# Kernel optimization log

Hardware: AMD Instinct MI355X
Metric: run time of the kernel (lower is better)

## Reference

```python
import jax, jax.numpy as jnp
import numpy as np

B, ND, NK = 4096, 32, 64        # batch, num_drones, num_docks
FD, FK = 16, 16                  # nfeat_drone, nfeat_dock
NHID, H = 128, 4                 # hidden dim, attention heads
ALPHA = 0.2                      # leaky relu slope
NEG = -9e15                      # masking constant from torch code


def setup_inputs() -> dict:
    key = jax.random.key(0)
    ks = jax.random.split(key, 13)
    s = 0.1
    obs = jax.random.normal(ks[0], (B, ND * FD + NK * FK + ND * NK), jnp.float32)
    return {
        "obs": obs,
        # DroneDockGAT params (per-head projections + additive attention vectors)
        "W_drone": jax.random.normal(ks[1], (H, FD, NHID), jnp.float32) * s,
        "W_dock": jax.random.normal(ks[2], (H, FK, NHID), jnp.float32) * s,
        "a_src": jax.random.normal(ks[3], (H, NHID), jnp.float32) * s,
        "a_dst": jax.random.normal(ks[4], (H, NHID), jnp.float32) * s,
        # critic: Linear(nhid*num_drones,64) -> ReLU -> Linear(64,1)
        "Wc1": jax.random.normal(ks[5], (NHID * ND, 64), jnp.float32) * s,
        "bc1": jnp.zeros((64,), jnp.float32),
        "Wc2": jax.random.normal(ks[6], (64, 1), jnp.float32) * s,
        "bc2": jnp.zeros((1,), jnp.float32),
        # actor heads
        "Wad": jax.random.normal(ks[7], (NHID, NHID), jnp.float32) * s,
        "bad": jnp.zeros((NHID,), jnp.float32),
        "Wak": jax.random.normal(ks[8], (NHID, NHID), jnp.float32) * s,
        "bak": jnp.zeros((NHID,), jnp.float32),
    }


def reference(obs, W_drone, W_dock, a_src, a_dst, Wc1, bc1, Wc2, bc2, Wad, bad, Wak, bak):
    sd, sk = ND * FD, NK * FK
    drone = obs[:, :sd].reshape(B, ND, FD)
    dock = obs[:, sd:sd + sk].reshape(B, NK, FK)
    adj = obs[:, sd + sk:].reshape(B, ND, NK)

    # per-head projections: [B, H, ND, NHID] / [B, H, NK, NHID]
    Whd = jnp.einsum('bnf,hfk->bhnk', drone, W_drone)
    Whk = jnp.einsum('bmf,hfk->bhmk', dock, W_dock)

    # additive GAT attention scores e[b,h,n,m]
    e = jax.nn.leaky_relu(
        jnp.einsum('bhnk,hk->bhn', Whd, a_src)[:, :, :, None]
        + jnp.einsum('bhmk,hk->bhm', Whk, a_dst)[:, :, None, :],
        ALPHA,
    )
    e = jnp.where(adj[:, None, :, :] > 0, e, NEG)
    attn = jax.nn.softmax(e, axis=-1)

    # head-averaged outputs with ELU
    h_drone = jax.nn.elu(jnp.einsum('bhnm,bhmk->bnk', attn, Whk) / H)  # [B, ND, NHID]
    h_dock = jax.nn.elu(Whk.mean(axis=1))                               # [B, NK, NHID]

    # critic
    values = jax.nn.relu(h_drone.reshape(B, -1) @ Wc1 + bc1) @ Wc2 + bc2  # [B, 1]

    # actor: masked drone-dock score matrix
    q = h_drone @ Wad + bad
    k = h_dock @ Wak + bak
    scores = jnp.einsum('bnk,bmk->bnm', q, k)
    logits = jnp.where(adj > 0, scores, NEG)  # [B, ND, NK]
    return values, logits
```

## Files before the change

### kernel.cpp

```cpp
#include <hip/hip_runtime.h>
#include <math.h>

#define OBSD 3584
#define NEGC -9e15f

typedef short short8 __attribute__((ext_vector_type(8)));
typedef float float4v __attribute__((ext_vector_type(4)));

#define WS_MT_S   0
#define WS_U_F    8192
#define WS_W_F    8320
#define WS_C0_F   8448
#define WS_AW_F   8452
#define WS_WDMT_S 17160
#define WS_WFT_S  19208

__device__ __forceinline__ float elu_f(float x) {
    return x > 0.f ? x : (__expf(x) - 1.f);
}
__device__ __forceinline__ short f2bf(float f) {
    union { float f; unsigned u; } v; v.f = f;
    unsigned u = v.u;
    unsigned r = (u + 0x7fffu + ((u >> 16) & 1u)) >> 16;
    return (short)r;
}
__device__ __forceinline__ float b2f(short s) {
    union { unsigned u; float f; } v; v.u = ((unsigned)(unsigned short)s) << 16;
    return v.f;
}
__device__ __forceinline__ unsigned pk2(float a, float b) {
    return (unsigned)(unsigned short)f2bf(a) | ((unsigned)(unsigned short)f2bf(b) << 16);
}

__global__ __launch_bounds__(256) void setup_fold(
    const float* __restrict__ W_drone, const float* __restrict__ W_dock,
    const float* __restrict__ a_src, const float* __restrict__ a_dst,
    const float* __restrict__ Wad, const float* __restrict__ Wak,
    const float* __restrict__ bad, const float* __restrict__ bak,
    float* __restrict__ wsf, short* __restrict__ wss)
{
    const int t = threadIdx.x, bi = blockIdx.x;
    if (bi < 16) {
        __shared__ float sa[32 * 132];
        __shared__ float sb[32 * 132];
        const int r0 = (bi >> 2) * 32, i0 = (bi & 3) * 32;
        #pragma unroll
        for (int qq = 0; qq < 4; ++qq) {
            int e = (t + 256 * qq) * 4;
            int r = e >> 7, cc = e & 127;
            *(float4*)&sa[r * 132 + cc] = *(const float4*)&Wad[(r0 + r) * 128 + cc];
            *(float4*)&sb[r * 132 + cc] = *(const float4*)&Wak[(i0 + r) * 128 + cc];
        }
        __syncthreads();
        int rr = (t >> 4) * 2, ii = (t & 15) * 2;
        float a00 = 0.f, a01 = 0.f, a10 = 0.f, a11 = 0.f;
        for (int c = 0; c < 128; ++c) {
            float x0 = sa[rr * 132 + c], x1 = sa[(rr + 1) * 132 + c];
            float y0 = sb[ii * 132 + c], y1 = sb[(ii + 1) * 132 + c];
            a00 += x0 * y0; a01 += x0 * y1; a10 += x1 * y0; a11 += x1 * y1;
        }
        wss[WS_MT_S + (i0 + ii) * 128 + (r0 + rr)]         = f2bf(a00);
        wss[WS_MT_S + (i0 + ii + 1) * 128 + (r0 + rr)]     = f2bf(a01);
        wss[WS_MT_S + (i0 + ii) * 128 + (r0 + rr + 1)]     = f2bf(a10);
        wss[WS_MT_S + (i0 + ii + 1) * 128 + (r0 + rr + 1)] = f2bf(a11);
    } else if (bi == 16) {
        if (t < 128) {
            float acc = 0.f;
            for (int c = 0; c < 128; ++c) acc += Wad[t * 128 + c] * bak[c];
            wsf[WS_U_F + t] = acc;
        } else {
            int j = t - 128;
            float acc = 0.f;
            for (int c = 0; c < 128; ++c) acc += Wak[j * 128 + c] * bad[c];
            wsf[WS_W_F + j] = acc;
        }
        if (t == 0) {
            float acc = 0.f;
            for (int c = 0; c < 128; ++c) acc += bad[c] * bak[c];
            wsf[WS_C0_F] = acc;
        }
    } else {
        if (t < 64) {
            int h = t >> 4, f = t & 15;
            const float* wrow = W_drone + h * 2048 + f * 128;
            const float* arow = a_src + h * 128;
            float acc = 0.f;
            for (int k = 0; k < 128; ++k) acc += wrow[k] * arow[k];
            wsf[WS_AW_F + t] = acc;
        } else if (t < 128) {
            int tt = t - 64;
            int h = tt >> 4, f = tt & 15;
            const float* wrow = W_dock + h * 2048 + f * 128;
            const float* arow = a_dst + h * 128;
            float acc = 0.f;
            for (int k = 0; k < 128; ++k) acc += wrow[k] * arow[k];
            wsf[WS_AW_F + 64 + tt] = acc;
        }
        for (int idx = t; idx < 2048; idx += 256) {
            int k2 = idx >> 4, f = idx & 15;
            float v = 0.25f * (W_dock[f * 128 + k2] + W_dock[2048 + f * 128 + k2]
                             + W_dock[4096 + f * 128 + k2] + W_dock[6144 + f * 128 + k2]);
            wss[WS_WDMT_S + k2 * 16 + f] = f2bf(v);
        }
        for (int idx = t; idx < 8192; idx += 256) {
            int k2 = idx >> 6, f64 = idx & 63;
            float v = W_dock[(f64 >> 4) * 2048 + (f64 & 15) * 128 + k2];
            wss[WS_WFT_S + k2 * 64 + f64] = f2bf(v);
        }
    }
}

__global__ __launch_bounds__(256, 2) void k1_attn_hd(
    const float* __restrict__ obs,
    const float* __restrict__ wsf, const short* __restrict__ wss,
    short* __restrict__ hdg)
{
    __shared__ __align__(16) char sm[57856];
    short* sD   = (short*)(sm + 0);
    short* sK   = (short*)(sm + 1024);
    short* sAdj = (short*)(sm + 3072);
    float* sAw  = (float*)(sm + 7680);
    float* sSrc = (float*)(sm + 8192);
    float* sDst = (float*)(sm + 8704);
    short* sAt  = (short*)(sm + 9728);
    short* sT   = (short*)(sm + 28160);
    short* sHd  = (short*)(sm + 32768);
    short* sWf  = (short*)(sm + 41472);

    const int t = threadIdx.x;
    const int b = blockIdx.x;
    const float* obsrow = obs + (size_t)b * OBSD;
    const int L = t & 63, c = L & 15, q = L >> 4, w = t >> 6;

    #pragma unroll
    for (int i = 0; i < 4; ++i) {
        int q4 = t + 256 * i;
        if (q4 < 896) {
            float4 v = ((const float4*)obsrow)[q4];
            int e0 = q4 * 4;
            if (e0 < 512) {
                int n = e0 >> 4, f0 = e0 & 15;
                sD[(f0 + 0) * 32 + n] = f2bf(v.x);
                sD[(f0 + 1) * 32 + n] = f2bf(v.y);
                sD[(f0 + 2) * 32 + n] = f2bf(v.z);
                sD[(f0 + 3) * 32 + n] = f2bf(v.w);
            } else if (e0 < 1536) {
                int e = e0 - 512;
                int m = e >> 4, f0 = e & 15;
                sK[(f0 + 0) * 64 + m] = f2bf(v.x);
                sK[(f0 + 1) * 64 + m] = f2bf(v.y);
                sK[(f0 + 2) * 64 + m] = f2bf(v.z);
                sK[(f0 + 3) * 64 + m] = f2bf(v.w);
            } else {
                int e = e0 - 1536;
                int n = e >> 6, m0 = e & 63;
                uint2 pkd = { pk2(v.x, v.y), pk2(v.z, v.w) };
                *(uint2*)&sAdj[n * 72 + m0] = pkd;
            }
        }
    }
    #pragma unroll
    for (int i = 0; i < 4; ++i)
        ((uint4*)sWf)[t + 256 * i] = ((const uint4*)(wss + WS_WFT_S))[t + 256 * i];
    if (t < 128) sAw[t] = wsf[WS_AW_F + t];
    __syncthreads();

    if (t < 128) {
        int h = t >> 5, n = t & 31;
        float acc = 0.f;
        #pragma unroll
        for (int f = 0; f < 16; ++f) acc += b2f(sD[f * 32 + n]) * sAw[h * 16 + f];
        sSrc[h * 32 + n] = acc;
    }
    {
        int h = t >> 6, m = t & 63;
        float acc = 0.f;
        #pragma unroll
        for (int f = 0; f < 16; ++f) acc += b2f(sK[f * 64 + m]) * sAw[64 + h * 16 + f];
        sDst[h * 64 + m] = acc;
    }
    __syncthreads();

    {
        int row = t >> 1, j = t & 1;
        int h = row >> 5, n = row & 31, m0 = j * 32;
        float sv = sSrc[h * 32 + n];
        float e32[32];
        float pmax = -INFINITY;
        #pragma unroll
        for (int mm = 0; mm < 32; ++mm) {
            int m = m0 + mm;
            float e = sv + sDst[h * 64 + m];
            e = e > 0.f ? e : 0.2f * e;
            e = (b2f(sAdj[n * 72 + m]) > 0.f) ? e : NEGC;
            e32[mm] = e;
            pmax = fmaxf(pmax, e);
        }
        pmax = fmaxf(pmax, __shfl_xor(pmax, 1, 2));
        float psum = 0.f;
        #pragma unroll
        for (int mm = 0; mm < 32; ++mm) { e32[mm] = __expf(e32[mm] - pmax); psum += e32[mm]; }
        psum += __shfl_xor(psum, 1, 2);
        float rinv = 1.f / psum;
        unsigned* ab = (unsigned*)sAt;
        int ub = (h * 2304 + n * 72 + m0) >> 1;
        #pragma unroll
        for (int mm = 0; mm < 32; mm += 2)
            ab[ub + (mm >> 1)] = pk2(e32[mm] * rinv, e32[mm + 1] * rinv);
    }
    __syncthreads();

    {
        int h = w;
        float4v accT[2] = { {0,0,0,0}, {0,0,0,0} };
        #pragma unroll
        for (int mt = 0; mt < 2; ++mt)
            #pragma unroll
            for (int kq = 0; kq < 2; ++kq) {
                short8 a = *(const short8*)&sAt[h * 2304 + (mt * 16 + c) * 72 + kq * 32 + q * 8];
                short8 bb = *(const short8*)&sK[c * 64 + kq * 32 + q * 8];
                accT[mt] = __builtin_amdgcn_mfma_f32_16x16x32_bf16(a, bb, accT[mt], 0, 0, 0);
            }
        #pragma unroll
        for (int mt = 0; mt < 2; ++mt)
            #pragma unroll
            for (int i = 0; i < 4; ++i)
                sT[(mt * 16 + q * 4 + i) * 72 + h * 16 + c] = f2bf(accT[mt][i]);
    }
    __syncthreads();

    {
        int mt = w & 1, ntb = (w >> 1) * 4;
        float4v acc[4] = { {0,0,0,0}, {0,0,0,0}, {0,0,0,0}, {0,0,0,0} };
        #pragma unroll
        for (int kq = 0; kq < 2; ++kq) {
            short8 a = *(const short8*)&sT[(mt * 16 + c) * 72 + kq * 32 + q * 8];
            #pragma unroll
            for (int p = 0; p < 4; ++p) {
                short8 bb = *(const short8*)&sWf[((ntb + p) * 16 + c) * 64 + kq * 32 + q * 8];
                acc[p] = __builtin_amdgcn_mfma_f32_16x16x32_bf16(a, bb, acc[p], 0, 0, 0);
            }
        }
        #pragma unroll
        for (int p = 0; p < 4; ++p)
            #pragma unroll
            for (int i = 0; i < 4; ++i) {
                float v = elu_f(acc[p][i] * 0.25f);
                sHd[(mt * 16 + q * 4 + i) * 136 + (ntb + p) * 16 + c] = f2bf(v);
            }
    }
    __syncthreads();

    {
        int n = t >> 3, k2 = (t & 7) * 16;
        uint4 x0 = *(const uint4*)&sHd[n * 136 + k2];
        uint4 x1 = *(const uint4*)&sHd[n * 136 + k2 + 8];
        uint4* dst = (uint4*)(hdg + (size_t)b * 4096 + n * 128 + k2);
        dst[0] = x0; dst[1] = x1;
    }
}

__global__ __launch_bounds__(256) void k2_critic(
    const short* __restrict__ hdg,
    const float* __restrict__ Wc1, const float* __restrict__ bc1,
    const float* __restrict__ Wc2, const float* __restrict__ bc2,
    float* __restrict__ out_values)
{
    __shared__ __align__(16) char sm[46592];
    short* As   = (short*)(sm + 0);
    float* Wst  = (float*)(sm + 9216);
    short* Bh   = (short*)(sm + 27648);
    short* Blo  = (short*)(sm + 36864);
    float* bc1L = (float*)(sm + 46080);
    float* wc2L = (float*)(sm + 46336);

    const int t = threadIdx.x;
    const int r0 = blockIdx.x * 64;
    const int L = t & 63, c = L & 15, q = L >> 4, w = t >> 6;

    if (t < 64) { bc1L[t] = bc1[t]; wc2L[t] = Wc2[t]; }

    float4v acc[4] = { {0,0,0,0}, {0,0,0,0}, {0,0,0,0}, {0,0,0,0} };

    for (int kc = 0; kc < 64; ++kc) {
        __syncthreads();
        {
            int r = t >> 2, kk0 = (t & 3) * 16;
            const uint4* src = (const uint4*)(hdg + (size_t)(r0 + r) * 4096 + kc * 64 + kk0);
            *(uint4*)&As[r * 72 + kk0]     = src[0];
            *(uint4*)&As[r * 72 + kk0 + 8] = src[1];
        }
        {
            int el = t >> 2, j0 = (t & 3) * 16;
            const float4* src = (const float4*)&Wc1[(size_t)(kc * 64 + el) * 64 + j0];
            #pragma unroll
            for (int u = 0; u < 4; ++u)
                *(float4*)&Wst[el * 72 + j0 + 4 * u] = src[u];
        }
        __syncthreads();
        {
            int j = t & 63, elb = (t >> 6) * 16;
            #pragma unroll
            for (int e = 0; e < 16; e += 2) {
                float v0 = Wst[(elb + e) * 72 + j];
                float v1 = Wst[(elb + e + 1) * 72 + j];
                short h0 = f2bf(v0), h1 = f2bf(v1);
                float l0 = v0 - b2f(h0), l1 = v1 - b2f(h1);
                *(unsigned*)&Bh[j * 72 + elb + e]  = (unsigned)(unsigned short)h0 | ((unsigned)(unsigned short)h1 << 16);
                *(unsigned*)&Blo[j * 72 + elb + e] = (unsigned)(unsigned short)f2bf(l0) | ((unsigned)(unsigned short)f2bf(l1) << 16);
            }
        }
        __syncthreads();
        #pragma unroll
        for (int kq = 0; kq < 2; ++kq) {
            short8 a = *(const short8*)&As[(w * 16 + c) * 72 + kq * 32 + q * 8];
            #pragma unroll
            for (int ct = 0; ct < 4; ++ct) {
                short8 bh = *(const short8*)&Bh[(ct * 16 + c) * 72 + kq * 32 + q * 8];
                short8 bl = *(const short8*)&Blo[(ct * 16 + c) * 72 + kq * 32 + q * 8];
                acc[ct] = __builtin_amdgcn_mfma_f32_16x16x32_bf16(a, bh, acc[ct], 0, 0, 0);
                acc[ct] = __builtin_amdgcn_mfma_f32_16x16x32_bf16(a, bl, acc[ct], 0, 0, 0);
            }
        }
    }
    float bc2v = bc2[0];
    #pragma unroll
    for (int i = 0; i < 4; ++i) {
        float sv = 0.f;
        #pragma unroll
        for (int ct = 0; ct < 4; ++ct) {
            float pre = acc[ct][i] + bc1L[ct * 16 + c];
            pre = fmaxf(pre, 0.f);
            sv += pre * wc2L[ct * 16 + c];
        }
        sv += __shfl_xor(sv, 1, 16);
        sv += __shfl_xor(sv, 2, 16);
        sv += __shfl_xor(sv, 4, 16);
        sv += __shfl_xor(sv, 8, 16);
        if (c == 0) out_values[r0 + w * 16 + q * 4 + i] = sv + bc2v;
    }
}

__global__ __launch_bounds__(256, 2) void k3_logits(
    const float* __restrict__ obs,
    const float* __restrict__ wsf, const short* __restrict__ wss,
    float* __restrict__ out_logits)
{
    __shared__ __align__(16) char sm[75648];
    short* dockRm = (short*)(sm + 0);
    short* adjBf  = (short*)(sm + 2048);
    short* hdS    = (short*)(sm + 6656);
    short* hkS    = (short*)(sm + 15360);
    short* wdmTS  = (short*)(sm + 32768);
    short* t2S    = (short*)(sm + 32768);
    float* suL    = (float*)(sm + 41472);
    float* swL    = (float*)(sm + 41600);
    float* uL     = (float*)(sm + 41856);
    float* wL     = (float*)(sm + 42368);
    short* MtS    = (short*)(sm + 42880);

    const int t = threadIdx.x;
    const int b = blockIdx.x;
    const float* obsrow = obs + (size_t)b * OBSD;
    short* hdg = (short*)out_logits;
    const int L = t & 63, c = L & 15, q = L >> 4, w = t >> 6;

    {
        int n = t >> 3, k2 = (t & 7) * 16;
        const uint4* src = (const uint4*)(hdg + (size_t)b * 4096 + n * 128 + k2);
        uint4 x0 = src[0], x1 = src[1];
        *(uint4*)&hdS[n * 136 + k2]     = x0;
        *(uint4*)&hdS[n * 136 + k2 + 8] = x1;
    }
    {
        float4 v = ((const float4*)obsrow)[128 + t];
        int m = t >> 2, f0 = (t & 3) * 4;
        uint2 pkd = { pk2(v.x, v.y), pk2(v.z, v.w) };
        *(uint2*)&dockRm[m * 16 + f0] = pkd;
    }
    #pragma unroll
    for (int i = 0; i < 2; ++i) {
        int q4 = 384 + t + 256 * i;
        if (q4 < 896) {
            float4 v = ((const float4*)obsrow)[q4];
            int e = q4 * 4 - 1536;
            int n = e >> 6, m0 = e & 63;
            uint2 pkd = { pk2(v.x, v.y), pk2(v.z, v.w) };
            *(uint2*)&adjBf[n * 72 + m0] = pkd;
        }
    }
    ((uint4*)wdmTS)[t] = ((const uint4*)(wss + WS_WDMT_S))[t];
    #pragma unroll
    for (int i = 0; i < 8; ++i)
        ((uint4*)MtS)[t + 256 * i] = ((const uint4*)(wss + WS_MT_S))[t + 256 * i];
    if (t < 128) uL[t] = wsf[WS_U_F + t];
    else wL[t - 128] = wsf[WS_W_F + (t - 128)];
    __syncthreads();

    {
        int mt = w;
        short8 a;
        if (q < 2) a = *(const short8*)&dockRm[(mt * 16 + c) * 16 + q * 8];
        else a = short8{0, 0, 0, 0, 0, 0, 0, 0};
        float swp[4] = {0.f, 0.f, 0.f, 0.f};
        #pragma unroll
        for (int nt = 0; nt < 8; ++nt) {
            short8 bb;
            if (q < 2) bb = *(const short8*)&wdmTS[(nt * 16 + c) * 16 + q * 8];
            else bb = short8{0, 0, 0, 0, 0, 0, 0, 0};
            float4v acc = {0, 0, 0, 0};
            acc = __builtin_amdgcn_mfma_f32_16x16x32_bf16(a, bb, acc, 0, 0, 0);
            float wv = wL[nt * 16 + c];
            #pragma unroll
            for (int i = 0; i < 4; ++i) {
                float ev = elu_f(acc[i]);
                hkS[(mt * 16 + q * 4 + i) * 136 + nt * 16 + c] = f2bf(ev);
                swp[i] += ev * wv;
            }
        }
        #pragma unroll
        for (int i = 0; i < 4; ++i) {
            float sv = swp[i];
            sv += __shfl_xor(sv, 1, 16);
            sv += __shfl_xor(sv, 2, 16);
            sv += __shfl_xor(sv, 4, 16);
            sv += __shfl_xor(sv, 8, 16);
            if (c == 0) swL[mt * 16 + q * 4 + i] = sv;
        }
    }
    {
        int n = t >> 3, p = t & 7;
        float a = 0.f;
        #pragma unroll
        for (int kk = 0; kk < 16; kk += 2) {
            unsigned uu = *(const unsigned*)&hdS[n * 136 + p * 16 + kk];
            a += b2f((short)(uu & 0xffff)) * uL[p * 16 + kk]
               + b2f((short)(uu >> 16))   * uL[p * 16 + kk + 1];
        }
        a += __shfl_xor(a, 1, 8);
        a += __shfl_xor(a, 2, 8);
        a += __shfl_xor(a, 4, 8);
        if (p == 0) suL[n] = a;
    }
    __syncthreads();

    {
        int mt = w & 1, ntb = (w >> 1) * 4;
        float4v acc[4] = { {0,0,0,0}, {0,0,0,0}, {0,0,0,0}, {0,0,0,0} };
        #pragma unroll
        for (int kq = 0; kq < 4; ++kq) {
            short8 a = *(const short8*)&hdS[(mt * 16 + c) * 136 + kq * 32 + q * 8];
            #pragma unroll
            for (int p = 0; p < 4; ++p) {
                short8 bb = *(const short8*)&MtS[((ntb + p) * 16 + c) * 128 + kq * 32 + q * 8];
                acc[p] = __builtin_amdgcn_mfma_f32_16x16x32_bf16(a, bb, acc[p], 0, 0, 0);
            }
        }
        __syncthreads();
        #pragma unroll
        for (int p = 0; p < 4; ++p)
            #pragma unroll
            for (int i = 0; i < 4; ++i)
                t2S[(mt * 16 + q * 4 + i) * 136 + (ntb + p) * 16 + c] = f2bf(acc[p][i]);
    }
    __syncthreads();

    {
        const float c0v = wsf[WS_C0_F];
        int ntd = w;
        float* lg = out_logits + (size_t)b * 2048;
        #pragma unroll
        for (int mt = 0; mt < 2; ++mt) {
            float4v acc = {0, 0, 0, 0};
            #pragma unroll
            for (int kq = 0; kq < 4; ++kq) {
                short8 a  = *(const short8*)&t2S[(mt * 16 + c) * 136 + kq * 32 + q * 8];
                short8 bb = *(const short8*)&hkS[(ntd * 16 + c) * 136 + kq * 32 + q * 8];
                acc = __builtin_amdgcn_mfma_f32_16x16x32_bf16(a, bb, acc, 0, 0, 0);
            }
            int col = ntd * 16 + c;
            float swv = swL[col];
            #pragma unroll
            for (int i = 0; i < 4; ++i) {
                int row = mt * 16 + q * 4 + i;
                float val = acc[i] + suL[row] + swv + c0v;
                bool keep = b2f(adjBf[row * 72 + col]) > 0.f;
                lg[row * 64 + col] = keep ? val : NEGC;
            }
        }
    }
}

extern "C" void kernel_launch(void* const* d_in, const int* in_sizes, int n_in,
                              void* d_out, int out_size, void* d_ws, size_t ws_size,
                              hipStream_t stream) {
    (void)in_sizes; (void)n_in; (void)out_size; (void)ws_size;
    const float* obs     = (const float*)d_in[0];
    const float* W_drone = (const float*)d_in[1];
    const float* W_dock  = (const float*)d_in[2];
    const float* a_src   = (const float*)d_in[3];
    const float* a_dst   = (const float*)d_in[4];
    const float* Wc1     = (const float*)d_in[5];
    const float* bc1     = (const float*)d_in[6];
    const float* Wc2     = (const float*)d_in[7];
    const float* bc2     = (const float*)d_in[8];
    const float* Wad     = (const float*)d_in[9];
    const float* bad     = (const float*)d_in[10];
    const float* Wak     = (const float*)d_in[11];
    const float* bak     = (const float*)d_in[12];
    float* out = (float*)d_out;
    float* wsf = (float*)d_ws;
    short* wss = (short*)d_ws;
    short* hdg = (short*)(out + 4096);

    setup_fold<<<dim3(18), dim3(256), 0, stream>>>(
        W_drone, W_dock, a_src, a_dst, Wad, Wak, bad, bak, wsf, wss);
    k1_attn_hd<<<dim3(4096), dim3(256), 0, stream>>>(obs, wsf, wss, hdg);
    k2_critic<<<dim3(64), dim3(256), 0, stream>>>(hdg, Wc1, bc1, Wc2, bc2, out);
    k3_logits<<<dim3(4096), dim3(256), 0, stream>>>(obs, wsf, wss, out + 4096);
}
```

Measured before the change: 309.9 us.

## Pre-split Wc1 into bf16 hi/lo and widen critic GEMM grid

Adds a setup kernel that transposes Wc1 and splits it into bf16 high and low parts in workspace. A new critic kernel uses 256 blocks of 16 rows each instead of 64 blocks and runs two MFMAs per step (hi and lo) to keep near-fp32 accuracy. The goal is better GPU occupancy for the critic GEMM and dropping on-the-fly fp32 weight conversion. The new path is taken only when the workspace is large enough, otherwise the old kernel runs.

```diff
diff --git a/kernel.cpp b/kernel.cpp
--- a/kernel.cpp
+++ b/kernel.cpp
@@ -14,6 +14,9 @@
 #define WS_AW_F   8452
 #define WS_WDMT_S 17160
 #define WS_WFT_S  19208
+#define WS_WC1H_S 32768
+#define WS_WC1L_S 294912
+#define WS_NEED_BYTES 1114112ull
 
 __device__ __forceinline__ float elu_f(float x) {
     return x > 0.f ? x : (__expf(x) - 1.f);
@@ -107,6 +110,20 @@
             float v = W_dock[(f64 >> 4) * 2048 + (f64 & 15) * 128 + k2];
             wss[WS_WFT_S + k2 * 64 + f64] = f2bf(v);
         }
+    }
+}
+
+__global__ __launch_bounds__(256) void setup_wc1(
+    const float* __restrict__ Wc1,
+    short* __restrict__ wc1h, short* __restrict__ wc1l)
+{
+    const int col = blockIdx.x;
+    for (int k = threadIdx.x; k < 4096; k += 256) {
+        float v = Wc1[(size_t)k * 64 + col];
+        short hi = f2bf(v);
+        float lo = v - b2f(hi);
+        wc1h[col * 4096 + k] = hi;
+        wc1l[col * 4096 + k] = f2bf(lo);
     }
 }
 
@@ -341,6 +358,74 @@
     }
 }
 
+__global__ __launch_bounds__(256) void k2_critic2(
+    const short* __restrict__ hdg,
+    const short* __restrict__ wc1h, const short* __restrict__ wc1l,
+    const float* __restrict__ bc1,
+    const float* __restrict__ Wc2, const float* __restrict__ bc2,
+    float* __restrict__ out_values)
+{
+    __shared__ __align__(16) char sm[39936];
+    short* As   = (short*)(sm + 0);
+    short* Bh   = (short*)(sm + 4352);
+    short* Bl   = (short*)(sm + 21760);
+    float* bc1L = (float*)(sm + 39168);
+    float* wc2L = (float*)(sm + 39424);
+    float* red  = (float*)(sm + 39680);
+
+    const int t = threadIdx.x;
+    const int r0 = blockIdx.x * 16;
+    const int L = t & 63, c = L & 15, q = L >> 4, w = t >> 6;
+
+    if (t < 64) { bc1L[t] = bc1[t]; wc2L[t] = Wc2[t]; }
+
+    float4v acc = {0, 0, 0, 0};
+
+    const int rA  = t >> 4,  kkA = (t & 15) * 8;
+    const int colB = t >> 2, kbB = (t & 3) * 32;
+
+    for (int it = 0; it < 32; ++it) {
+        const int kc = it * 128;
+        __syncthreads();
+        *(uint4*)&As[rA * 136 + kkA] =
+            *(const uint4*)(hdg + (size_t)(r0 + rA) * 4096 + kc + kkA);
+        {
+            const uint4* srcH = (const uint4*)(wc1h + (size_t)colB * 4096 + kc + kbB);
+            const uint4* srcL = (const uint4*)(wc1l + (size_t)colB * 4096 + kc + kbB);
+            #pragma unroll
+            for (int u = 0; u < 4; ++u) {
+                *(uint4*)&Bh[colB * 136 + kbB + 8 * u] = srcH[u];
+                *(uint4*)&Bl[colB * 136 + kbB + 8 * u] = srcL[u];
+            }
+        }
+        __syncthreads();
+        #pragma unroll
+        for (int kq = 0; kq < 4; ++kq) {
+            short8 a  = *(const short8*)&As[c * 136 + kq * 32 + q * 8];
+            short8 bh = *(const short8*)&Bh[(w * 16 + c) * 136 + kq * 32 + q * 8];
+            short8 bl = *(const short8*)&Bl[(w * 16 + c) * 136 + kq * 32 + q * 8];
+            acc = __builtin_amdgcn_mfma_f32_16x16x32_bf16(a, bh, acc, 0, 0, 0);
+            acc = __builtin_amdgcn_mfma_f32_16x16x32_bf16(a, bl, acc, 0, 0, 0);
+        }
+    }
+    #pragma unroll
+    for (int i = 0; i < 4; ++i) {
+        float pre = acc[i] + bc1L[w * 16 + c];
+        pre = fmaxf(pre, 0.f);
+        float sv = pre * wc2L[w * 16 + c];
+        sv += __shfl_xor(sv, 1, 16);
+        sv += __shfl_xor(sv, 2, 16);
+        sv += __shfl_xor(sv, 4, 16);
+        sv += __shfl_xor(sv, 8, 16);
+        if (c == 0) red[w * 16 + q * 4 + i] = sv;
+    }
+    __syncthreads();
+    if (t < 16) {
+        float v = red[t] + red[16 + t] + red[32 + t] + red[48 + t] + bc2[0];
+        out_values[r0 + t] = v;
+    }
+}
+
 __global__ __launch_bounds__(256, 2) void k3_logits(
     const float* __restrict__ obs,
     const float* __restrict__ wsf, const short* __restrict__ wss,
@@ -494,7 +579,7 @@
 extern "C" void kernel_launch(void* const* d_in, const int* in_sizes, int n_in,
                               void* d_out, int out_size, void* d_ws, size_t ws_size,
                               hipStream_t stream) {
-    (void)in_sizes; (void)n_in; (void)out_size; (void)ws_size;
+    (void)in_sizes; (void)n_in; (void)out_size;
     const float* obs     = (const float*)d_in[0];
     const float* W_drone = (const float*)d_in[1];
     const float* W_dock  = (const float*)d_in[2];
@@ -513,9 +598,21 @@
     short* wss = (short*)d_ws;
     short* hdg = (short*)(out + 4096);
 
+    const bool big_ws = (ws_size >= WS_NEED_BYTES);
+
     setup_fold<<<dim3(18), dim3(256), 0, stream>>>(
         W_drone, W_dock, a_src, a_dst, Wad, Wak, bad, bak, wsf, wss);
+    if (big_ws)
+        setup_wc1<<<dim3(64), dim3(256), 0, stream>>>(
+            Wc1, wss + WS_WC1H_S, wss + WS_WC1L_S);
+
     k1_attn_hd<<<dim3(4096), dim3(256), 0, stream>>>(obs, wsf, wss, hdg);
-    k2_critic<<<dim3(64), dim3(256), 0, stream>>>(hdg, Wc1, bc1, Wc2, bc2, out);
+
+    if (big_ws)
+        k2_critic2<<<dim3(256), dim3(256), 0, stream>>>(
+            hdg, wss + WS_WC1H_S, wss + WS_WC1L_S, bc1, Wc2, bc2, out);
+    else
+        k2_critic<<<dim3(64), dim3(256), 0, stream>>>(hdg, Wc1, bc1, Wc2, bc2, out);
+
     k3_logits<<<dim3(4096), dim3(256), 0, stream>>>(obs, wsf, wss, out + 4096);
 }
```

New measurement: 263.3 us. 1.18x faster.
